# Kernel tuning notes

Hardware: AMD Instinct MI355X
Metric: run time of the kernel (lower is better)

Reference implementation:

```python
import jax, jax.numpy as jnp
import numpy as np

IN_DIM, HID, MID, FFN, OUT = 384, 128, 1024, 512, 1024
B, T = 8, 4096
LN_EPS = 1e-5


def _legs_hippo(n: int) -> np.ndarray:
    # A[i, j] = P_i(2j/n - 1) * sqrt(2i + 1), Legendre via 3-term recurrence
    x = 2.0 * np.arange(n) / n - 1.0          # eval points, shape [n]
    P = np.zeros((n, n), dtype=np.float64)     # P[i] = P_i(x)
    P[0] = 1.0
    if n > 1:
        P[1] = x
    for i in range(1, n - 1):
        P[i + 1] = ((2 * i + 1) * x * P[i] - i * P[i - 1]) / (i + 1)
    A = P * np.sqrt(2.0 * np.arange(n) + 1.0)[:, None]
    # rescale so the 4096-step recurrence stays finite (A is a free Parameter,
    # so any test value is valid; unscaled LegS overflows fp32 in ~20 steps)
    s = np.linalg.norm(A, 2)
    return (A / (1.05 * s)).astype(np.float32)


def _layernorm(x, g, b):
    mu = jnp.mean(x, axis=-1, keepdims=True)
    var = jnp.var(x, axis=-1, keepdims=True)
    return (x - mu) * jax.lax.rsqrt(var + LN_EPS) * g + b


def setup_inputs() -> dict:
    key = jax.random.key(0)
    ks = jax.random.split(key, 16)

    def w(k, shape, fan_in):
        return jax.random.normal(k, shape, jnp.float32) * (1.0 / np.sqrt(fan_in))

    return {
        "padded_x": jax.random.normal(ks[0], (B, T, IN_DIM), jnp.float32),
        "seq_lens": jax.random.randint(ks[1], (B,), 1, T + 1, jnp.int32),
        "A": jnp.asarray(_legs_hippo(HID)),
        "enc_w1": w(ks[2], (IN_DIM, MID), IN_DIM), "enc_b1": jnp.zeros((MID,), jnp.float32),
        "enc_w2": w(ks[3], (MID, HID), MID), "enc_b2": jnp.zeros((HID,), jnp.float32),
        "proj_w": w(ks[4], (HID, MID), HID), "proj_b": jnp.zeros((MID,), jnp.float32),
        "ln1_g": jnp.ones((MID,), jnp.float32), "ln1_b": jnp.zeros((MID,), jnp.float32),
        "ffn_w1": w(ks[5], (MID, FFN), MID), "ffn_b1": jnp.zeros((FFN,), jnp.float32),
        "ffn_w2": w(ks[6], (FFN, OUT), FFN), "ffn_b2": jnp.zeros((OUT,), jnp.float32),
        "ln2_g": jnp.ones((OUT,), jnp.float32), "ln2_b": jnp.zeros((OUT,), jnp.float32),
        "out_w": w(ks[7], (OUT, OUT), OUT), "out_b": jnp.zeros((OUT,), jnp.float32),
    }


def reference(padded_x, seq_lens, A, enc_w1, enc_b1, enc_w2, enc_b2,
              proj_w, proj_b, ln1_g, ln1_b, ffn_w1, ffn_b1, ffn_w2, ffn_b2,
              ln2_g, ln2_b, out_w, out_b):
    # encoder: Linear -> GELU(exact) -> Linear   [B, T, HID]
    h_mid = jax.nn.gelu(padded_x @ enc_w1 + enc_b1, approximate=False)
    seqs_bx = h_mid @ enc_w2 + enc_b2

    # masked linear recurrence h_t = A @ h_{t-1} + Bx_t via lax.scan over time
    xs = jnp.swapaxes(seqs_bx, 0, 1)           # [T, B, HID]
    ts = jnp.arange(xs.shape[0])

    def step(h, inp):
        x_t, t = inp
        upd = h @ A.T + x_t                     # (A @ h)^T batched
        mask = (t < seq_lens)[:, None]          # [B, 1]
        return jnp.where(mask, upd, h), None

    h0 = jnp.zeros((padded_x.shape[0], A.shape[0]), padded_x.dtype)
    batch_h, _ = jax.lax.scan(step, h0, (xs, ts))

    # decoder
    projected = batch_h @ proj_w + proj_b
    norm_h = _layernorm(projected, ln1_g, ln1_b)
    ffn_out = jax.nn.gelu(norm_h @ ffn_w1 + ffn_b1, approximate=False) @ ffn_w2 + ffn_b2
    ffn_out = ffn_out + projected               # residual (requires OUT == MID)
    norm_ffn = _layernorm(ffn_out, ln2_g, ln2_b)
    return norm_ffn @ out_w + out_b             # [B, OUT]
```

## Files before the change

kernel.cpp:

```cpp
#include <hip/hip_runtime.h>

typedef __attribute__((ext_vector_type(8))) short short8;
typedef __attribute__((ext_vector_type(4))) short short4v;
typedef __attribute__((ext_vector_type(4))) float float4v;

__device__ __forceinline__ float bf2f(short s) {
  union { float f; unsigned u; } cv; cv.u = ((unsigned)(unsigned short)s) << 16; return cv.f;
}
__device__ __forceinline__ short f2bf(float f) {
  union { float f; unsigned u; } cv; cv.f = f;
  unsigned u = cv.u;
  unsigned r = u + 0x7FFFu + ((u >> 16) & 1u);
  return (short)(r >> 16);
}
__device__ __forceinline__ float gelu_f(float v) {
  float ax = fabsf(v) * 0.70710678118654752440f;
  float t = __builtin_amdgcn_rcpf(__builtin_fmaf(0.3275911f, ax, 1.0f));
  float poly = __builtin_fmaf(t, 1.061405429f, -1.453152027f);
  poly = __builtin_fmaf(t, poly, 1.421413741f);
  poly = __builtin_fmaf(t, poly, -0.284496736f);
  poly = __builtin_fmaf(t, poly, 0.254829592f);
  poly *= t;
  float e = __expf(-ax * ax);
  float erfax = __builtin_fmaf(-poly, e, 1.0f);
  float erfx = (v < 0.0f) ? -erfax : erfax;
  return 0.5f * v * (1.0f + erfx);
}
__device__ __forceinline__ void glds16(const short* g, short* l) {
  __builtin_amdgcn_global_load_lds(
      (const __attribute__((address_space(1))) void*)g,
      (__attribute__((address_space(3))) void*)l, 16, 0, 0);
}

__global__ __launch_bounds__(256) void enc_fused(
    const short* __restrict__ xB, const short* __restrict__ w1T,
    const short* __restrict__ w2T, const float* __restrict__ b1,
    float* __restrict__ encP, const int* __restrict__ seq_lens)
{
  int m0 = blockIdx.x * 64;
  { int b = m0 >> 12, t = m0 & 4095; if (t >= seq_lens[b]) return; }
  int nc0 = blockIdx.y * 2;

  __shared__ __align__(16) short As[64 * 64];
  __shared__ __align__(16) short Ws[128 * 64];
  __shared__ __align__(16) short midb[64 * 128];

  int tid = threadIdx.x, lane = tid & 63, wave = tid >> 6;
  int l15 = lane & 15, quad = lane >> 4;
  int lr = lane >> 3, lseg = lane & 7;

  float4v accO[4][2];
#pragma unroll
  for (int i = 0; i < 4; i++)
#pragma unroll
    for (int j = 0; j < 2; j++) accO[i][j] = 0;

  for (int nci = 0; nci < 2; ++nci) {
    int nc = nc0 + nci;
    float4v accM[4][2];
#pragma unroll
    for (int i = 0; i < 4; i++)
#pragma unroll
      for (int j = 0; j < 2; j++) accM[i][j] = 0;

    for (int ks = 0; ks < 6; ++ks) {
      int kk = ks * 64;
#pragma unroll
      for (int i = 0; i < 2; i++) {
        int rowg = wave * 16 + i * 8;
        glds16(xB + (size_t)(m0 + rowg + lr) * 384 + kk + (lseg ^ lr) * 8, &As[rowg * 64]);
      }
#pragma unroll
      for (int i = 0; i < 4; i++) {
        int rowg = wave * 32 + i * 8;
        glds16(w1T + (size_t)(nc * 128 + rowg + lr) * 384 + kk + (lseg ^ lr) * 8, &Ws[rowg * 64]);
      }
      __syncthreads();
#pragma unroll
      for (int kh = 0; kh < 2; kh++) {
        int s = kh * 4 + quad;
        short8 af[4], bfr[2];
#pragma unroll
        for (int im = 0; im < 4; im++) {
          int r = im * 16 + l15;
          af[im] = *(short8*)&As[r * 64 + ((s ^ (r & 7)) * 8)];
        }
#pragma unroll
        for (int in = 0; in < 2; in++) {
          int r = wave * 32 + in * 16 + l15;
          bfr[in] = *(short8*)&Ws[r * 64 + ((s ^ (r & 7)) * 8)];
        }
#pragma unroll
        for (int im = 0; im < 4; im++)
#pragma unroll
          for (int in = 0; in < 2; in++)
            accM[im][in] = __builtin_amdgcn_mfma_f32_16x16x32_bf16(af[im], bfr[in], accM[im][in], 0, 0, 0);
      }
      __syncthreads();
    }
#pragma unroll
    for (int in = 0; in < 2; in++) {
      int k = wave * 32 + in * 16 + l15;
      float bias = b1[nc * 128 + k];
      int s = k >> 3, kb = k & 7;
#pragma unroll
      for (int im = 0; im < 4; im++)
#pragma unroll
        for (int reg = 0; reg < 4; reg++) {
          int m = im * 16 + quad * 4 + reg;
          float v = gelu_f(accM[im][in][reg] + bias);
          int sw = (s & 8) | ((s & 7) ^ (m & 7));
          midb[m * 128 + sw * 8 + kb] = f2bf(v);
        }
    }
    __syncthreads();
#pragma unroll
    for (int ks2 = 0; ks2 < 2; ++ks2) {
      int kk = nc * 128 + ks2 * 64;
#pragma unroll
      for (int i = 0; i < 4; i++) {
        int rowg = wave * 32 + i * 8;
        glds16(w2T + (size_t)(rowg + lr) * 1024 + kk + (lseg ^ lr) * 8, &Ws[rowg * 64]);
      }
      __syncthreads();
#pragma unroll
      for (int kh = 0; kh < 2; kh++) {
        short8 af[4], bfr[2];
#pragma unroll
        for (int im = 0; im < 4; im++) {
          int m = im * 16 + l15;
          int kb = ks2 * 64 + kh * 32 + quad * 8;
          int s = kb >> 3;
          int sw = (s & 8) | ((s & 7) ^ (m & 7));
          af[im] = *(short8*)&midb[m * 128 + sw * 8];
        }
#pragma unroll
        for (int in = 0; in < 2; in++) {
          int r = wave * 32 + in * 16 + l15;
          int s = kh * 4 + quad;
          bfr[in] = *(short8*)&Ws[r * 64 + ((s ^ (r & 7)) * 8)];
        }
#pragma unroll
        for (int im = 0; im < 4; im++)
#pragma unroll
          for (int in = 0; in < 2; in++)
            accO[im][in] = __builtin_amdgcn_mfma_f32_16x16x32_bf16(af[im], bfr[in], accO[im][in], 0, 0, 0);
      }
      __syncthreads();
    }
  }
  float* outp = encP + ((size_t)blockIdx.y << 22);
#pragma unroll
  for (int im = 0; im < 4; im++)
#pragma unroll
    for (int in = 0; in < 2; in++) {
      int n = wave * 32 + in * 16 + l15;
#pragma unroll
      for (int reg = 0; reg < 4; reg++) {
        int m = m0 + im * 16 + quad * 4 + reg;
        outp[(size_t)m * 128 + n] = accO[im][in][reg];
      }
    }
}

__global__ __launch_bounds__(256) void enc_reduce(
    const float* __restrict__ encP, const float* __restrict__ b2,
    short* __restrict__ seqs, const int* __restrict__ seq_lens,
    const short* __restrict__ Spow, const short* __restrict__ SpowT,
    short* __restrict__ P1, short* __restrict__ P1t, short* __restrict__ P2t)
{
  __shared__ short cur[16384];
  if (blockIdx.x >= 512) {
    int bid = blockIdx.x - 512;
    int table1 = bid < 63 ? 1 : 0;
    int e = table1 ? bid + 1 : bid - 62;
    int t = threadIdx.x, lane = t & 63, wave = t >> 6;
    int l15 = lane & 15, quad = lane >> 4;
    int bits = e;
    int k0 = __ffs(bits) - 1; bits &= bits - 1;
    int s0 = table1 ? k0 : (k0 == 0 ? 6 : 6 + k0);
    for (int i = t * 8; i < 16384; i += 2048)
      *(short8*)&cur[i] = *(const short8*)&Spow[(size_t)s0 * 16384 + i];
    while (bits) {
      int k = __ffs(bits) - 1; bits &= bits - 1;
      int si = table1 ? k : (k == 0 ? 6 : 6 + k);
      const short* Bt = SpowT + (size_t)si * 16384;
      __syncthreads();
      float4v acc[2][8];
#pragma unroll
      for (int mt = 0; mt < 2; mt++)
#pragma unroll
        for (int nt = 0; nt < 8; nt++) acc[mt][nt] = 0;
#pragma unroll 1
      for (int ks = 0; ks < 4; ++ks) {
        short8 af0 = *(short8*)&cur[(wave * 32 + l15) * 128 + ks * 32 + quad * 8];
        short8 af1 = *(short8*)&cur[(wave * 32 + 16 + l15) * 128 + ks * 32 + quad * 8];
#pragma unroll
        for (int nt = 0; nt < 8; ++nt) {
          short8 bf = *(const short8*)&Bt[(nt * 16 + l15) * 128 + ks * 32 + quad * 8];
          acc[0][nt] = __builtin_amdgcn_mfma_f32_16x16x32_bf16(af0, bf, acc[0][nt], 0, 0, 0);
          acc[1][nt] = __builtin_amdgcn_mfma_f32_16x16x32_bf16(af1, bf, acc[1][nt], 0, 0, 0);
        }
      }
      __syncthreads();
#pragma unroll
      for (int mt = 0; mt < 2; ++mt)
#pragma unroll
        for (int nt = 0; nt < 8; ++nt)
#pragma unroll
          for (int reg = 0; reg < 4; ++reg) {
            int m = wave * 32 + mt * 16 + quad * 4 + reg;
            int n = nt * 16 + l15;
            cur[m * 128 + n] = f2bf(acc[mt][nt][reg]);
          }
    }
    __syncthreads();
    int slot = 63 - e;
    for (int idx = t; idx < 16384; idx += 256) {
      int i = idx >> 7, j = idx & 127;
      short v = cur[idx];
      if (table1) {
        P1[i * 8192 + slot * 128 + j] = v;
        P1t[(slot * 128 + j) * 128 + i] = v;
      } else {
        P2t[(slot * 128 + j) * 128 + i] = v;
      }
    }
    return;
  }

  int m0 = blockIdx.x * 64;
  { int b = m0 >> 12, t = m0 & 4095; if (t >= seq_lens[b]) return; }
  int t = threadIdx.x;
#pragma unroll
  for (int i = 0; i < 8; i++) {
    int f4 = t + i * 256;
    int m = m0 + (f4 >> 5);
    int cg = f4 & 31;
    size_t off = (size_t)m * 128 + cg * 4;
    float4v v = *(const float4v*)&encP[off];
#pragma unroll
    for (int y = 1; y < 4; y++) {
      float4v w = *(const float4v*)&encP[((size_t)y << 22) + off];
#pragma unroll
      for (int q = 0; q < 4; q++) v[q] += w[q];
    }
    float4v bb = *(const float4v*)&b2[cg * 4];
    short4v o;
#pragma unroll
    for (int q = 0; q < 4; q++) o[q] = f2bf(v[q] + bb[q]);
    *(short4v*)&seqs[off] = o;
  }
}

__global__ __launch_bounds__(256) void gemm_bt(
    const short* __restrict__ A_, const short* __restrict__ BT,
    float* __restrict__ out, int lda, int ldb, int ldc,
    int kSteps, int kChunk)
{
  int m0 = blockIdx.y * 128;
  int n0 = blockIdx.x * 128;
  int kBase = blockIdx.z * kChunk;

  __shared__ __align__(16) short As[128 * 64];
  __shared__ __align__(16) short Bs[128 * 64];

  int tid = threadIdx.x;
  int lane = tid & 63, wave = tid >> 6;
  int l15 = lane & 15, quad = lane >> 4;
  int wm = wave & 1, wn = wave >> 1;
  int lr = lane >> 3, lseg = lane & 7;

  float4v acc[4][4];
#pragma unroll
  for (int i = 0; i < 4; i++)
#pragma unroll
    for (int j = 0; j < 4; j++) acc[i][j] = 0;

  for (int ks = 0; ks < kSteps; ++ks) {
    int kk = kBase + ks * 64;
#pragma unroll
    for (int i = 0; i < 4; i++) {
      int rowg = wave * 32 + i * 8;
      glds16(A_ + (size_t)(m0 + rowg + lr) * lda + kk + (lseg ^ lr) * 8, &As[rowg * 64]);
      glds16(BT + (size_t)(n0 + rowg + lr) * ldb + kk + (lseg ^ lr) * 8, &Bs[rowg * 64]);
    }
    __syncthreads();
#pragma unroll
    for (int kh = 0; kh < 2; kh++) {
      int s = kh * 4 + quad;
      short8 af[4], bfr[4];
#pragma unroll
      for (int im = 0; im < 4; im++) {
        int r = wm * 64 + im * 16 + l15;
        af[im] = *(short8*)&As[r * 64 + ((s ^ (r & 7)) * 8)];
      }
#pragma unroll
      for (int in = 0; in < 4; in++) {
        int r = wn * 64 + in * 16 + l15;
        bfr[in] = *(short8*)&Bs[r * 64 + ((s ^ (r & 7)) * 8)];
      }
#pragma unroll
      for (int im = 0; im < 4; im++)
#pragma unroll
        for (int in = 0; in < 4; in++)
          acc[im][in] = __builtin_amdgcn_mfma_f32_16x16x32_bf16(af[im], bfr[in], acc[im][in], 0, 0, 0);
    }
    __syncthreads();
  }
  float* outz = out + (size_t)blockIdx.z * 65536;
#pragma unroll
  for (int im = 0; im < 4; im++)
#pragma unroll
    for (int in = 0; in < 4; in++) {
      int n = n0 + wn * 64 + in * 16 + l15;
#pragma unroll
      for (int reg = 0; reg < 4; reg++) {
        int m = m0 + wm * 64 + im * 16 + quad * 4 + reg;
        outz[(size_t)m * ldc + n] = acc[im][in][reg];
      }
    }
}

__global__ void prep_wide(const float* __restrict__ x, const float* __restrict__ w1,
                          const float* __restrict__ w2,
                          const float* __restrict__ proj_w, const float* __restrict__ ffn_w1,
                          const float* __restrict__ ffn_w2, const float* __restrict__ out_w,
                          const float* __restrict__ A, const int* __restrict__ seq_lens,
                          short* __restrict__ xB,
                          short* __restrict__ w1T, short* __restrict__ w2T,
                          short* __restrict__ projB, short* __restrict__ ffn1B,
                          short* __restrict__ ffn2B, short* __restrict__ outB,
                          short* __restrict__ P1, short* __restrict__ P1t,
                          short* __restrict__ P2t,
                          short* __restrict__ Spow, short* __restrict__ SpowT)
{
  __shared__ short X[16384];
  __shared__ short XT[16384];
  if (blockIdx.x == 23104) {
    int t = threadIdx.x;
    for (int i = t; i < 16384; i += 256) X[i] = f2bf(A[i]);
    for (int i = t; i < 16384; i += 256) {
      int j = i >> 7, r = i & 127;
      XT[i] = f2bf(A[r * 128 + j]);
    }
    __syncthreads();
    int lane = t & 63, wave = t >> 6, l15 = lane & 15, quad = lane >> 4;
    for (int step = 1; step <= 11; ++step) {
      float4v acc[2][8];
#pragma unroll
      for (int mt = 0; mt < 2; mt++)
#pragma unroll
        for (int nt = 0; nt < 8; nt++) acc[mt][nt] = 0;
#pragma unroll 1
      for (int ks = 0; ks < 4; ++ks) {
        short8 af0 = *(short8*)&X[(wave * 32 + l15) * 128 + ks * 32 + quad * 8];
        short8 af1 = *(short8*)&X[(wave * 32 + 16 + l15) * 128 + ks * 32 + quad * 8];
#pragma unroll
        for (int nt = 0; nt < 8; ++nt) {
          short8 bf = *(short8*)&XT[(nt * 16 + l15) * 128 + ks * 32 + quad * 8];
          acc[0][nt] = __builtin_amdgcn_mfma_f32_16x16x32_bf16(af0, bf, acc[0][nt], 0, 0, 0);
          acc[1][nt] = __builtin_amdgcn_mfma_f32_16x16x32_bf16(af1, bf, acc[1][nt], 0, 0, 0);
        }
      }
      __syncthreads();
      short* gX  = Spow  + (size_t)step * 16384;
      short* gXT = SpowT + (size_t)step * 16384;
#pragma unroll
      for (int mt = 0; mt < 2; ++mt)
#pragma unroll
        for (int nt = 0; nt < 8; ++nt) {
          int mb = wave * 32 + mt * 16 + quad * 4;
          int n = nt * 16 + l15;
          short4v o;
#pragma unroll
          for (int reg = 0; reg < 4; ++reg) {
            short v = f2bf(acc[mt][nt][reg]);
            X[(mb + reg) * 128 + n] = v;
            gX[(mb + reg) * 128 + n] = v;
            o[reg] = v;
          }
          *(short4v*)&XT[n * 128 + mb] = o;
          *(short4v*)&gXT[(size_t)n * 128 + mb] = o;
        }
      __syncthreads();
    }
    return;
  }

  int idx = blockIdx.x * 256 + threadIdx.x;
  if (idx < 3145728) {
    int row = idx / 96;
    int t = row & 4095, b = row >> 12;
    if (t >= seq_lens[b]) return;
    float4v v = ((const float4v*)x)[idx];
    short4v o;
#pragma unroll
    for (int j = 0; j < 4; j++) o[j] = f2bf(v[j]);
    ((short4v*)xB)[idx] = o;
    return;
  }
  idx -= 3145728;
  if (idx < 393216) {
    int n = idx / 384, k = idx % 384;
    w1T[idx] = f2bf(w1[k * 1024 + n]);
    return;
  }
  idx -= 393216;
  if (idx < 131072) {
    int n = idx / 1024, k = idx % 1024;
    w2T[idx] = f2bf(w2[k * 128 + n]);
    return;
  }
  idx -= 131072;
  if (idx < 131072) { projB[idx] = f2bf(proj_w[idx]); return; }
  idx -= 131072;
  if (idx < 524288) { ffn1B[idx] = f2bf(ffn_w1[idx]); return; }
  idx -= 524288;
  if (idx < 524288) { ffn2B[idx] = f2bf(ffn_w2[idx]); return; }
  idx -= 524288;
  if (idx < 1048576) { outB[idx] = f2bf(out_w[idx]); return; }
  idx -= 1048576;
  if (idx < 16384) {
    int i = idx >> 7, j = idx & 127;
    short bidv = f2bf((i == j) ? 1.0f : 0.0f);
    P1[i * 8192 + 63 * 128 + j] = bidv;
    P1t[(63 * 128 + j) * 128 + i] = bidv;
    P2t[(63 * 128 + j) * 128 + i] = bidv;
    short ab = f2bf(A[idx]);
    Spow[idx] = ab;
    SpowT[(size_t)j * 128 + i] = ab;
  }
}

__global__ __launch_bounds__(256) void combine_gemm(
    const float* __restrict__ Vz, const short* __restrict__ seqs,
    const int* __restrict__ seq_lens,
    const short* __restrict__ P2t, const short* __restrict__ P1t,
    float* __restrict__ hFtail)
{
  __shared__ short X[256 * 8];
  int pp = blockIdx.x >> 5, ks = blockIdx.x & 31;
  int t = threadIdx.x;
  for (int e = t; e < 2048; e += 256) {
    int klocal = e >> 3, b = e & 7;
    int cp = ks * 2 + (klocal >> 7), i = klocal & 127;
    int L = seq_lens[b];
    if (pp == 0) {
      int F = L >> 6, sh = 64 - F;
      float v = 0.f;
      if (cp >= sh) {
        int row = (b * 64 + (cp - sh)) * 128 + i;
#pragma unroll
        for (int z = 0; z < 32; z++) v += Vz[(size_t)z * 65536 + row];
      }
      X[e] = f2bf(v);
    } else {
      int F = L >> 6, rr = L & 63, sh = 64 - rr;
      short s = 0;
      if (cp >= sh) s = seqs[((size_t)b * 4096 + F * 64 + (cp - sh)) * 128 + i];
      X[e] = s;
    }
  }
  __syncthreads();
  const short* P = pp ? P1t : P2t;
  float* outp = hFtail + pp * 1024;
  int i = t & 127, g = t >> 7;
  float acc[4] = {0, 0, 0, 0};
  for (int kl = 0; kl < 256; ++kl) {
    int k = ks * 256 + kl;
    float pv = bf2f(P[k * 128 + i]);
    short4v xv = *(const short4v*)(X + kl * 8 + g * 4);
#pragma unroll
    for (int q = 0; q < 4; q++) acc[q] += bf2f(xv[q]) * pv;
  }
#pragma unroll
  for (int q = 0; q < 4; q++) atomicAdd(&outp[(g * 4 + q) * 128 + i], acc[q]);
}

__global__ __launch_bounds__(256) void proj_stage(
    const float* __restrict__ hFtail, const short* __restrict__ P1t,
    const int* __restrict__ seq_lens, const short* __restrict__ projB,
    const float* __restrict__ proj_b, float* __restrict__ projected)
{
  __shared__ short hT[128 * 8];
  __shared__ float red[4][64][8];
  int t = threadIdx.x;
  {
    int b = t >> 5, i4 = (t & 31) * 4;
    int rr = seq_lens[b] & 63;
    const short* M = P1t + (size_t)(63 - rr) * 128 * 128;
    const float* hF = hFtail + b * 128;
    float acc[4];
#pragma unroll
    for (int q = 0; q < 4; q++) acc[q] = hFtail[1024 + b * 128 + i4 + q];
    for (int j = 0; j < 128; ++j) {
      float hv = hF[j];
      short4v mv = *(const short4v*)&M[j * 128 + i4];
#pragma unroll
      for (int q = 0; q < 4; q++) acc[q] += bf2f(mv[q]) * hv;
    }
#pragma unroll
    for (int q = 0; q < 4; q++) hT[(i4 + q) * 8 + b] = f2bf(acc[q]);
  }
  __syncthreads();
  int c = t & 63, sl = t >> 6;
  int n = blockIdx.x * 64 + c;
  float acc[8] = {0, 0, 0, 0, 0, 0, 0, 0};
  for (int k = sl * 32; k < sl * 32 + 32; ++k) {
    short8 xv = *(short8*)&hT[k * 8];
    float wv = bf2f(projB[k * 1024 + n]);
#pragma unroll
    for (int b = 0; b < 8; b++) acc[b] += bf2f(xv[b]) * wv;
  }
#pragma unroll
  for (int b = 0; b < 8; b++) red[sl][c][b] = acc[b];
  __syncthreads();
  if (sl == 0) {
#pragma unroll
    for (int s = 1; s < 4; s++)
#pragma unroll
      for (int b = 0; b < 8; b++) acc[b] += red[s][c][b];
    float bn = proj_b[n];
#pragma unroll
    for (int b = 0; b < 8; b++) projected[b * 1024 + n] = acc[b] + bn;
  }
}

__global__ __launch_bounds__(256) void ffn1_stage(
    const float* __restrict__ projected, const float* __restrict__ g1,
    const float* __restrict__ b1, const short* __restrict__ ffn1B,
    float* __restrict__ ffn1raw)
{
  __shared__ float part[8][32][2];
  __shared__ float stats[8][2];
  __shared__ short xT[256 * 8];
  __shared__ float red[4][64][8];
  int t = threadIdx.x;
  { int b = t >> 5, j0 = t & 31; float s = 0, q = 0;
    for (int k = j0 * 32; k < j0 * 32 + 32; ++k) { float v = projected[b * 1024 + k]; s += v; q += v * v; }
    part[b][j0][0] = s; part[b][j0][1] = q; }
  __syncthreads();
  if (t < 8) {
    float s = 0, q = 0;
    for (int j = 0; j < 32; j++) { s += part[t][j][0]; q += part[t][j][1]; }
    float mu = s * (1.0f / 1024.0f);
    float var = q * (1.0f / 1024.0f) - mu * mu;
    stats[t][0] = mu; stats[t][1] = rsqrtf(var + 1e-5f);
  }
  __syncthreads();
  int ky0 = blockIdx.y * 256;
  for (int idx = t; idx < 2048; idx += 256) {
    int kl = idx >> 3, b = idx & 7; int k = ky0 + kl;
    float v = (projected[b * 1024 + k] - stats[b][0]) * stats[b][1] * g1[k] + b1[k];
    xT[kl * 8 + b] = f2bf(v);
  }
  __syncthreads();
  int c = t & 63, sl = t >> 6;
  int n = blockIdx.x * 64 + c;
  float acc[8] = {0, 0, 0, 0, 0, 0, 0, 0};
  for (int kl = sl * 64; kl < sl * 64 + 64; ++kl) {
    short8 xv = *(short8*)&xT[kl * 8];
    float wv = bf2f(ffn1B[(size_t)(ky0 + kl) * 512 + n]);
#pragma unroll
    for (int b = 0; b < 8; b++) acc[b] += bf2f(xv[b]) * wv;
  }
#pragma unroll
  for (int b = 0; b < 8; b++) red[sl][c][b] = acc[b];
  __syncthreads();
  if (sl == 0) {
#pragma unroll
    for (int s = 1; s < 4; s++)
#pragma unroll
      for (int b = 0; b < 8; b++) acc[b] += red[s][c][b];
#pragma unroll
    for (int b = 0; b < 8; b++) atomicAdd(&ffn1raw[b * 512 + n], acc[b]);
  }
}

__global__ __launch_bounds__(256) void ffn2_stage(
    const float* __restrict__ ffn1raw, const float* __restrict__ fb1,
    const short* __restrict__ ffn2B, float* __restrict__ ffn2raw)
{
  __shared__ short xT[256 * 8];
  __shared__ float red[4][64][8];
  int t = threadIdx.x;
  int ky0 = blockIdx.y * 256;
  for (int idx = t; idx < 2048; idx += 256) {
    int kl = idx >> 3, b = idx & 7; int k = ky0 + kl;
    float v = gelu_f(ffn1raw[b * 512 + k] + fb1[k]);
    xT[kl * 8 + b] = f2bf(v);
  }
  __syncthreads();
  int c = t & 63, sl = t >> 6;
  int n = blockIdx.x * 64 + c;
  float acc[8] = {0, 0, 0, 0, 0, 0, 0, 0};
  for (int kl = sl * 64; kl < sl * 64 + 64; ++kl) {
    short8 xv = *(short8*)&xT[kl * 8];
    float wv = bf2f(ffn2B[(size_t)(ky0 + kl) * 1024 + n]);
#pragma unroll
    for (int b = 0; b < 8; b++) acc[b] += bf2f(xv[b]) * wv;
  }
#pragma unroll
  for (int b = 0; b < 8; b++) red[sl][c][b] = acc[b];
  __syncthreads();
  if (sl == 0) {
#pragma unroll
    for (int s = 1; s < 4; s++)
#pragma unroll
      for (int b = 0; b < 8; b++) acc[b] += red[s][c][b];
#pragma unroll
    for (int b = 0; b < 8; b++) atomicAdd(&ffn2raw[b * 1024 + n], acc[b]);
  }
}

__global__ __launch_bounds__(256) void out_stage(
    const float* __restrict__ ffn2raw, const float* __restrict__ fb2,
    const float* __restrict__ projected, const float* __restrict__ g2,
    const float* __restrict__ b2ln, const short* __restrict__ outB,
    const float* __restrict__ out_b, float* __restrict__ d_out)
{
  __shared__ float part[8][32][2];
  __shared__ float stats[8][2];
  __shared__ short xT[512 * 8];
  __shared__ float red[4][64][8];
  int t = threadIdx.x;
  { int b = t >> 5, j0 = t & 31; float s = 0, q = 0;
    for (int k = j0 * 32; k < j0 * 32 + 32; ++k) {
      float v = ffn2raw[b * 1024 + k] + fb2[k] + projected[b * 1024 + k];
      s += v; q += v * v;
    }
    part[b][j0][0] = s; part[b][j0][1] = q; }
  __syncthreads();
  if (t < 8) {
    float s = 0, q = 0;
    for (int j = 0; j < 32; j++) { s += part[t][j][0]; q += part[t][j][1]; }
    float mu = s * (1.0f / 1024.0f);
    float var = q * (1.0f / 1024.0f) - mu * mu;
    stats[t][0] = mu; stats[t][1] = rsqrtf(var + 1e-5f);
  }
  __syncthreads();
  int ky0 = blockIdx.y * 512;
  for (int idx = t; idx < 4096; idx += 256) {
    int kl = idx >> 3, b = idx & 7; int k = ky0 + kl;
    float v = ffn2raw[b * 1024 + k] + fb2[k] + projected[b * 1024 + k];
    v = (v - stats[b][0]) * stats[b][1] * g2[k] + b2ln[k];
    xT[kl * 8 + b] = f2bf(v);
  }
  __syncthreads();
  int c = t & 63, sl = t >> 6;
  int n = blockIdx.x * 64 + c;
  float acc[8] = {0, 0, 0, 0, 0, 0, 0, 0};
  for (int kl = sl * 128; kl < sl * 128 + 128; ++kl) {
    short8 xv = *(short8*)&xT[kl * 8];
    float wv = bf2f(outB[(size_t)(ky0 + kl) * 1024 + n]);
#pragma unroll
    for (int b = 0; b < 8; b++) acc[b] += bf2f(xv[b]) * wv;
  }
#pragma unroll
  for (int b = 0; b < 8; b++) red[sl][c][b] = acc[b];
  __syncthreads();
  if (sl == 0) {
#pragma unroll
    for (int s = 1; s < 4; s++)
#pragma unroll
      for (int b = 0; b < 8; b++) acc[b] += red[s][c][b];
    float bn = (blockIdx.y == 0) ? out_b[n] : 0.0f;
#pragma unroll
    for (int b = 0; b < 8; b++) atomicAdd(&d_out[b * 1024 + n], acc[b] + bn);
  }
}

extern "C" void kernel_launch(void* const* d_in, const int* in_sizes, int n_in,
                              void* d_out, int out_size, void* d_ws, size_t ws_size,
                              hipStream_t stream)
{
  (void)in_sizes; (void)n_in; (void)out_size; (void)ws_size;
  const float* x      = (const float*)d_in[0];
  const int* seq_lens = (const int*)d_in[1];
  const float* A      = (const float*)d_in[2];
  const float* enc_w1 = (const float*)d_in[3];
  const float* enc_b1 = (const float*)d_in[4];
  const float* enc_w2 = (const float*)d_in[5];
  const float* enc_b2 = (const float*)d_in[6];
  const float* proj_w = (const float*)d_in[7];
  const float* proj_b = (const float*)d_in[8];
  const float* ln1_g  = (const float*)d_in[9];
  const float* ln1_b  = (const float*)d_in[10];
  const float* ffn_w1 = (const float*)d_in[11];
  const float* ffn_b1 = (const float*)d_in[12];
  const float* ffn_w2 = (const float*)d_in[13];
  const float* ffn_b2 = (const float*)d_in[14];
  const float* ln2_g  = (const float*)d_in[15];
  const float* ln2_b  = (const float*)d_in[16];
  const float* out_w  = (const float*)d_in[17];
  const float* out_b  = (const float*)d_in[18];

  char* p = (char*)d_ws;
  auto alloc = [&](size_t bytes) { char* r = p; p += (bytes + 255) & ~(size_t)255; return r; };
  short* xB    = (short*)alloc(32768ull * 384 * 2);
  float* encP  = (float*)alloc(4ull * 32768 * 128 * 4);
  short* seqs  = (short*)alloc(32768ull * 128 * 2);
  short* w1T   = (short*)alloc(1024ull * 384 * 2);
  short* w2T   = (short*)alloc(128ull * 1024 * 2);
  short* projB = (short*)alloc(128ull * 1024 * 2);
  short* ffn1B = (short*)alloc(1024ull * 512 * 2);
  short* ffn2B = (short*)alloc(512ull * 1024 * 2);
  short* outB  = (short*)alloc(1024ull * 1024 * 2);
  short* Spow  = (short*)alloc(12ull * 16384 * 2);
  short* SpowT = (short*)alloc(12ull * 16384 * 2);
  short* P1    = (short*)alloc(128ull * 8192 * 2);
  short* P1t   = (short*)alloc(8192ull * 128 * 2);
  short* P2t   = (short*)alloc(8192ull * 128 * 2);
  float* Vz    = (float*)alloc(32ull * 512 * 128 * 4);
  float* hFtail  = (float*)alloc(2ull * 8 * 128 * 4);
  float* ffn1raw = (float*)alloc(8ull * 512 * 4);
  float* ffn2raw = (float*)alloc(8ull * 1024 * 4);
  float* projected = (float*)alloc(8ull * 1024 * 4);

  hipMemsetAsync(hFtail, 0, (2ull * 8 * 128 + 8ull * 512 + 8ull * 1024) * 4, stream);
  hipMemsetAsync(d_out, 0, 8192ull * 4, stream);

  prep_wide<<<23105, 256, 0, stream>>>(x, enc_w1, enc_w2, proj_w, ffn_w1, ffn_w2, out_w, A,
      seq_lens, xB, w1T, w2T, projB, ffn1B, ffn2B, outB, P1, P1t, P2t, Spow, SpowT);

  enc_fused<<<dim3(512, 4), 256, 0, stream>>>(xB, w1T, w2T, enc_b1, encP, seq_lens);
  enc_reduce<<<638, 256, 0, stream>>>(encP, enc_b2, seqs, seq_lens, Spow, SpowT, P1, P1t, P2t);

  gemm_bt<<<dim3(1, 4, 32), 256, 0, stream>>>(seqs, P1, Vz, 8192, 8192, 128, 4, 256);
  combine_gemm<<<64, 256, 0, stream>>>(Vz, seqs, seq_lens, P2t, P1t, hFtail);

  proj_stage<<<16, 256, 0, stream>>>(hFtail, P1t, seq_lens, projB, proj_b, projected);
  ffn1_stage<<<dim3(8, 4), 256, 0, stream>>>(projected, ln1_g, ln1_b, ffn1B, ffn1raw);
  ffn2_stage<<<dim3(16, 2), 256, 0, stream>>>(ffn1raw, ffn_b1, ffn2B, ffn2raw);
  out_stage<<<dim3(16, 2), 256, 0, stream>>>(ffn2raw, ffn_b2, projected, ln2_g, ln2_b,
      outB, out_b, (float*)d_out);
}
```

Baseline: 448.3 us.

## Compute matrix power tables independently per block inside prep kernel

Previously, one block in prep_wide computed 11 repeated squarings of A serially, and 126 blocks in enc_reduce then combined those powers into the P1/P1t/P2t tables. Now each of 126 prep_wide blocks computes its own power A^e by square-and-multiply, using a per-block global scratch buffer and device-scope atomic loads. This removes the serial dependency on the squaring chain and the extra blocks in enc_reduce. In exchange it repeats the squarings in every block and routes operands through global memory rather than LDS.

```diff
diff --git a/kernel.cpp b/kernel.cpp
--- a/kernel.cpp
+++ b/kernel.cpp
@@ -31,6 +31,59 @@
       (const __attribute__((address_space(1))) void*)g,
       (__attribute__((address_space(3))) void*)l, 16, 0, 0);
 }
+__device__ __forceinline__ short8 ld_dev(const short* p) {
+  union { short8 s; unsigned long long q[2]; } u;
+  u.q[0] = __hip_atomic_load((const unsigned long long*)p,     __ATOMIC_RELAXED, __HIP_MEMORY_SCOPE_AGENT);
+  u.q[1] = __hip_atomic_load(((const unsigned long long*)p) + 1, __ATOMIC_RELAXED, __HIP_MEMORY_SCOPE_AGENT);
+  return u.s;
+}
+
+__device__ void pow_mm(const short* __restrict__ P, const short* __restrict__ Qt,
+                       int mode, short* R, short* T,
+                       int table1, int slot,
+                       short* __restrict__ P1, short* __restrict__ P1t,
+                       short* __restrict__ P2t)
+{
+  int t = threadIdx.x, lane = t & 63, wave = t >> 6;
+  int l15 = lane & 15, quad = lane >> 4;
+#pragma unroll 1
+  for (int p = 0; p < 2; ++p) {
+    float4v acc[8];
+#pragma unroll
+    for (int nt = 0; nt < 8; ++nt) acc[nt] = 0;
+#pragma unroll 1
+    for (int ks = 0; ks < 4; ++ks) {
+      short8 af = ld_dev(&P[(wave * 32 + p * 16 + l15) * 128 + ks * 32 + quad * 8]);
+#pragma unroll
+      for (int nt = 0; nt < 8; ++nt) {
+        short8 bf = ld_dev(&Qt[(nt * 16 + l15) * 128 + ks * 32 + quad * 8]);
+        acc[nt] = __builtin_amdgcn_mfma_f32_16x16x32_bf16(af, bf, acc[nt], 0, 0, 0);
+      }
+    }
+    int mb = wave * 32 + p * 16 + quad * 4;
+#pragma unroll
+    for (int nt = 0; nt < 8; ++nt) {
+      int n = nt * 16 + l15;
+      short4v o;
+#pragma unroll
+      for (int reg = 0; reg < 4; ++reg) o[reg] = f2bf(acc[nt][reg]);
+      if (mode == 2) {
+        if (table1) {
+#pragma unroll
+          for (int reg = 0; reg < 4; ++reg) P1[(size_t)(mb + reg) * 8192 + slot * 128 + n] = o[reg];
+          *(short4v*)&P1t[((size_t)slot * 128 + n) * 128 + mb] = o;
+        } else {
+          *(short4v*)&P2t[((size_t)slot * 128 + n) * 128 + mb] = o;
+        }
+      } else {
+#pragma unroll
+        for (int reg = 0; reg < 4; ++reg) R[(mb + reg) * 128 + n] = o[reg];
+        if (mode == 0) *(short4v*)&T[n * 128 + mb] = o;
+      }
+    }
+  }
+  __syncthreads();
+}
 
 __global__ __launch_bounds__(256) void enc_fused(
     const short* __restrict__ xB, const short* __restrict__ w1T,
@@ -165,70 +218,8 @@
 
 __global__ __launch_bounds__(256) void enc_reduce(
     const float* __restrict__ encP, const float* __restrict__ b2,
-    short* __restrict__ seqs, const int* __restrict__ seq_lens,
-    const short* __restrict__ Spow, const short* __restrict__ SpowT,
-    short* __restrict__ P1, short* __restrict__ P1t, short* __restrict__ P2t)
-{
-  __shared__ short cur[16384];
-  if (blockIdx.x >= 512) {
-    int bid = blockIdx.x - 512;
-    int table1 = bid < 63 ? 1 : 0;
-    int e = table1 ? bid + 1 : bid - 62;
-    int t = threadIdx.x, lane = t & 63, wave = t >> 6;
-    int l15 = lane & 15, quad = lane >> 4;
-    int bits = e;
-    int k0 = __ffs(bits) - 1; bits &= bits - 1;
-    int s0 = table1 ? k0 : (k0 == 0 ? 6 : 6 + k0);
-    for (int i = t * 8; i < 16384; i += 2048)
-      *(short8*)&cur[i] = *(const short8*)&Spow[(size_t)s0 * 16384 + i];
-    while (bits) {
-      int k = __ffs(bits) - 1; bits &= bits - 1;
-      int si = table1 ? k : (k == 0 ? 6 : 6 + k);
-      const short* Bt = SpowT + (size_t)si * 16384;
-      __syncthreads();
-      float4v acc[2][8];
-#pragma unroll
-      for (int mt = 0; mt < 2; mt++)
-#pragma unroll
-        for (int nt = 0; nt < 8; nt++) acc[mt][nt] = 0;
-#pragma unroll 1
-      for (int ks = 0; ks < 4; ++ks) {
-        short8 af0 = *(short8*)&cur[(wave * 32 + l15) * 128 + ks * 32 + quad * 8];
-        short8 af1 = *(short8*)&cur[(wave * 32 + 16 + l15) * 128 + ks * 32 + quad * 8];
-#pragma unroll
-        for (int nt = 0; nt < 8; ++nt) {
-          short8 bf = *(const short8*)&Bt[(nt * 16 + l15) * 128 + ks * 32 + quad * 8];
-          acc[0][nt] = __builtin_amdgcn_mfma_f32_16x16x32_bf16(af0, bf, acc[0][nt], 0, 0, 0);
-          acc[1][nt] = __builtin_amdgcn_mfma_f32_16x16x32_bf16(af1, bf, acc[1][nt], 0, 0, 0);
-        }
-      }
-      __syncthreads();
-#pragma unroll
-      for (int mt = 0; mt < 2; ++mt)
-#pragma unroll
-        for (int nt = 0; nt < 8; ++nt)
-#pragma unroll
-          for (int reg = 0; reg < 4; ++reg) {
-            int m = wave * 32 + mt * 16 + quad * 4 + reg;
-            int n = nt * 16 + l15;
-            cur[m * 128 + n] = f2bf(acc[mt][nt][reg]);
-          }
-    }
-    __syncthreads();
-    int slot = 63 - e;
-    for (int idx = t; idx < 16384; idx += 256) {
-      int i = idx >> 7, j = idx & 127;
-      short v = cur[idx];
-      if (table1) {
-        P1[i * 8192 + slot * 128 + j] = v;
-        P1t[(slot * 128 + j) * 128 + i] = v;
-      } else {
-        P2t[(slot * 128 + j) * 128 + i] = v;
-      }
-    }
-    return;
-  }
-
+    short* __restrict__ seqs, const int* __restrict__ seq_lens)
+{
   int m0 = blockIdx.x * 64;
   { int b = m0 >> 12, t = m0 & 4095; if (t >= seq_lens[b]) return; }
   int t = threadIdx.x;
@@ -332,63 +323,65 @@
                           short* __restrict__ projB, short* __restrict__ ffn1B,
                           short* __restrict__ ffn2B, short* __restrict__ outB,
                           short* __restrict__ P1, short* __restrict__ P1t,
-                          short* __restrict__ P2t,
-                          short* __restrict__ Spow, short* __restrict__ SpowT)
-{
-  __shared__ short X[16384];
-  __shared__ short XT[16384];
-  if (blockIdx.x == 23104) {
+                          short* __restrict__ P2t, short* __restrict__ powScr)
+{
+  if (blockIdx.x < 126) {
     int t = threadIdx.x;
-    for (int i = t; i < 16384; i += 256) X[i] = f2bf(A[i]);
+    int table1 = blockIdx.x < 63;
+    int e = table1 ? blockIdx.x + 1 : blockIdx.x - 62;
+    int E = table1 ? e : (e << 6);
+    int slot = 63 - e;
+    int topbit = 31 - __clz(E);
+    short* base = powScr + (size_t)blockIdx.x * 6 * 16384;
+    short* curR[2] = {base,             base + 2 * 16384};
+    short* curT[2] = {base + 16384,     base + 3 * 16384};
+    short* resR[2] = {base + 4 * 16384, base + 5 * 16384};
     for (int i = t; i < 16384; i += 256) {
-      int j = i >> 7, r = i & 127;
-      XT[i] = f2bf(A[r * 128 + j]);
+      int r = i >> 7, j = i & 127;
+      short v = f2bf(A[i]);
+      curR[0][i] = v;
+      curT[0][(j << 7) + r] = v;
     }
     __syncthreads();
-    int lane = t & 63, wave = t >> 6, l15 = lane & 15, quad = lane >> 4;
-    for (int step = 1; step <= 11; ++step) {
-      float4v acc[2][8];
-#pragma unroll
-      for (int mt = 0; mt < 2; mt++)
-#pragma unroll
-        for (int nt = 0; nt < 8; nt++) acc[mt][nt] = 0;
-#pragma unroll 1
-      for (int ks = 0; ks < 4; ++ks) {
-        short8 af0 = *(short8*)&X[(wave * 32 + l15) * 128 + ks * 32 + quad * 8];
-        short8 af1 = *(short8*)&X[(wave * 32 + 16 + l15) * 128 + ks * 32 + quad * 8];
-#pragma unroll
-        for (int nt = 0; nt < 8; ++nt) {
-          short8 bf = *(short8*)&XT[(nt * 16 + l15) * 128 + ks * 32 + quad * 8];
-          acc[0][nt] = __builtin_amdgcn_mfma_f32_16x16x32_bf16(af0, bf, acc[0][nt], 0, 0, 0);
-          acc[1][nt] = __builtin_amdgcn_mfma_f32_16x16x32_bf16(af1, bf, acc[1][nt], 0, 0, 0);
+    int cb = 0, rb = 0, haveRes = 0;
+    for (int k = 0; k <= topbit; ++k) {
+      if ((E >> k) & 1) {
+        if (k == topbit) {
+          if (!haveRes) {
+            for (int idx = t * 8; idx < 16384; idx += 2048) {
+              short8 v = ld_dev(&curR[cb][idx]);
+              int i = idx >> 7, j0 = idx & 127;
+              if (table1) {
+                *(short8*)&P1[(size_t)i * 8192 + slot * 128 + j0] = v;
+#pragma unroll
+                for (int q = 0; q < 8; ++q) P1t[((size_t)slot * 128 + j0 + q) * 128 + i] = v[q];
+              } else {
+#pragma unroll
+                for (int q = 0; q < 8; ++q) P2t[((size_t)slot * 128 + j0 + q) * 128 + i] = v[q];
+              }
+            }
+          } else {
+            pow_mm(resR[rb], curT[cb], 2, nullptr, nullptr, table1, slot, P1, P1t, P2t);
+          }
+        } else if (!haveRes) {
+          for (int i = t * 8; i < 16384; i += 2048)
+            *(short8*)&resR[rb][i] = ld_dev(&curR[cb][i]);
+          haveRes = 1;
+          __syncthreads();
+        } else {
+          pow_mm(resR[rb], curT[cb], 1, resR[rb ^ 1], nullptr, 0, 0, nullptr, nullptr, nullptr);
+          rb ^= 1;
         }
       }
-      __syncthreads();
-      short* gX  = Spow  + (size_t)step * 16384;
-      short* gXT = SpowT + (size_t)step * 16384;
-#pragma unroll
-      for (int mt = 0; mt < 2; ++mt)
-#pragma unroll
-        for (int nt = 0; nt < 8; ++nt) {
-          int mb = wave * 32 + mt * 16 + quad * 4;
-          int n = nt * 16 + l15;
-          short4v o;
-#pragma unroll
-          for (int reg = 0; reg < 4; ++reg) {
-            short v = f2bf(acc[mt][nt][reg]);
-            X[(mb + reg) * 128 + n] = v;
-            gX[(mb + reg) * 128 + n] = v;
-            o[reg] = v;
-          }
-          *(short4v*)&XT[n * 128 + mb] = o;
-          *(short4v*)&gXT[(size_t)n * 128 + mb] = o;
-        }
-      __syncthreads();
+      if (k < topbit) {
+        pow_mm(curR[cb], curT[cb], 0, curR[cb ^ 1], curT[cb ^ 1], 0, 0, nullptr, nullptr, nullptr);
+        cb ^= 1;
+      }
     }
     return;
   }
 
-  int idx = blockIdx.x * 256 + threadIdx.x;
+  int idx = (blockIdx.x - 126) * 256 + threadIdx.x;
   if (idx < 3145728) {
     int row = idx / 96;
     int t = row & 4095, b = row >> 12;
@@ -427,9 +420,6 @@
     P1[i * 8192 + 63 * 128 + j] = bidv;
     P1t[(63 * 128 + j) * 128 + i] = bidv;
     P2t[(63 * 128 + j) * 128 + i] = bidv;
-    short ab = f2bf(A[idx]);
-    Spow[idx] = ab;
-    SpowT[(size_t)j * 128 + i] = ab;
   }
 }
 
@@ -707,11 +697,10 @@
   short* ffn1B = (short*)alloc(1024ull * 512 * 2);
   short* ffn2B = (short*)alloc(512ull * 1024 * 2);
   short* outB  = (short*)alloc(1024ull * 1024 * 2);
-  short* Spow  = (short*)alloc(12ull * 16384 * 2);
-  short* SpowT = (short*)alloc(12ull * 16384 * 2);
   short* P1    = (short*)alloc(128ull * 8192 * 2);
   short* P1t   = (short*)alloc(8192ull * 128 * 2);
   short* P2t   = (short*)alloc(8192ull * 128 * 2);
+  short* powScr= (short*)alloc(126ull * 6 * 16384 * 2);
   float* Vz    = (float*)alloc(32ull * 512 * 128 * 4);
   float* hFtail  = (float*)alloc(2ull * 8 * 128 * 4);
   float* ffn1raw = (float*)alloc(8ull * 512 * 4);
@@ -721,11 +710,11 @@
   hipMemsetAsync(hFtail, 0, (2ull * 8 * 128 + 8ull * 512 + 8ull * 1024) * 4, stream);
   hipMemsetAsync(d_out, 0, 8192ull * 4, stream);
 
-  prep_wide<<<23105, 256, 0, stream>>>(x, enc_w1, enc_w2, proj_w, ffn_w1, ffn_w2, out_w, A,
-      seq_lens, xB, w1T, w2T, projB, ffn1B, ffn2B, outB, P1, P1t, P2t, Spow, SpowT);
+  prep_wide<<<23230, 256, 0, stream>>>(x, enc_w1, enc_w2, proj_w, ffn_w1, ffn_w2, out_w, A,
+      seq_lens, xB, w1T, w2T, projB, ffn1B, ffn2B, outB, P1, P1t, P2t, powScr);
 
   enc_fused<<<dim3(512, 4), 256, 0, stream>>>(xB, w1T, w2T, enc_b1, encP, seq_lens);
-  enc_reduce<<<638, 256, 0, stream>>>(encP, enc_b2, seqs, seq_lens, Spow, SpowT, P1, P1t, P2t);
+  enc_reduce<<<512, 256, 0, stream>>>(encP, enc_b2, seqs, seq_lens);
 
   gemm_bt<<<dim3(1, 4, 32), 256, 0, stream>>>(seqs, P1, Vz, 8192, 8192, 128, 4, 256);
   combine_gemm<<<64, 256, 0, stream>>>(Vz, seqs, seq_lens, P2t, P1t, hFtail);
```

Result: slower. 588.8 us (+31.3%).
